# Kernel optimization log

Hardware: AMD Instinct MI355X
Metric: run time of the kernel (lower is better)

## Reference

```python
import jax, jax.numpy as jnp
import numpy as np

T, B, D_IN, D_H = 256, 256, 1024, 1024


def setup_inputs() -> dict:
    key = jax.random.key(0)
    k1, k2 = jax.random.split(key)
    seq = jax.random.normal(k1, (T, B, D_IN), dtype=jnp.float32)
    # Kaiming-ish init so tanh does not saturate
    W = jax.random.normal(k2, (D_H, D_IN + D_H), dtype=jnp.float32) / np.sqrt(D_IN + D_H)
    b = jnp.zeros((D_H,), dtype=jnp.float32)
    return {"seq": seq, "W": W, "b": b}


def reference(seq, W, b):
    # seq: (T, B, d_in); W: (d_h, d_in + d_h); b: (d_h,)
    d_h = W.shape[0]
    h0 = jnp.zeros((seq.shape[1], d_h), dtype=seq.dtype)

    def step(h, x):
        # h_{t+1} = tanh(W [h_t ; x_t] + b)
        h_new = jnp.tanh(jnp.concatenate([h, x], axis=-1) @ W.T + b)
        return h_new, h_new

    _, hs = jax.lax.scan(step, h0, seq)  # hs: (T, B, d_h)
    # Original returns the full hidden-state history including the initial zero state
    return jnp.concatenate([h0[None], hs], axis=0)  # (T+1, B, d_h)
```

## Files before the change

kernel.cpp:

```cpp
#include <hip/hip_runtime.h>

#define T_STEPS 256
#define BATCH   256
#define DIN     1024
#define DH      1024

typedef _Float16 half8_t __attribute__((ext_vector_type(8)));
typedef _Float16 half4_t __attribute__((ext_vector_type(4)));
typedef float    f32x4_t __attribute__((ext_vector_type(4)));

#define LDH  1032
#define REDW 68
#define LGW  72

#define CPOL_SYS 17

union H4U { half4_t h; unsigned long long u; };

__device__ __forceinline__ float ftanh(float x) {
    float t = x * 2.885390081777927f;
    float e = exp2f(t);
    float r = __builtin_amdgcn_rcpf(e + 1.0f);
    return 1.0f - 2.0f * r;
}

__global__ __launch_bounds__(256) void cvt_w(const float* __restrict__ W,
                                             _Float16* __restrict__ Wh,
                                             _Float16* __restrict__ Wx) {
    const int part = blockIdx.x >> 9;
    size_t base = ((size_t)(blockIdx.x & 511) * 256 + threadIdx.x) * 8;
    const int n = (int)(base >> 10);
    const int k = (int)(base & 1023);
    const float4* s = reinterpret_cast<const float4*>(W + (size_t)n * 2048 + part * 1024 + k);
    float4 a = s[0], b = s[1];
    half8_t h;
    h[0] = (_Float16)a.x; h[1] = (_Float16)a.y;
    h[2] = (_Float16)a.z; h[3] = (_Float16)a.w;
    h[4] = (_Float16)b.x; h[5] = (_Float16)b.y;
    h[6] = (_Float16)b.z; h[7] = (_Float16)b.w;
    _Float16* dst = part ? Wx : Wh;
    *reinterpret_cast<half8_t*>(dst + base) = h;
}

__global__ __launch_bounds__(256) void zero_h0(float* __restrict__ out,
                                               int* __restrict__ flags) {
    size_t i = (size_t)blockIdx.x * 256 + threadIdx.x;
    reinterpret_cast<float4*>(out)[i] = make_float4(0.f, 0.f, 0.f, 0.f);
    if (blockIdx.x == 0) {
#pragma unroll
        for (int j = 0; j < 16; ++j)
            __hip_atomic_store(&flags[(int)threadIdx.x * 16 + j], 0,
                               __ATOMIC_RELAXED, __HIP_MEMORY_SCOPE_SYSTEM);
    }
}

__global__ __launch_bounds__(256) void zgemm(const float* __restrict__ seq,
                                             const _Float16* __restrict__ Wx,
                                             const float* __restrict__ bias,
                                             float* __restrict__ out) {
    __shared__ __align__(16) _Float16 la[128 * LGW];
    __shared__ __align__(16) _Float16 lb[128 * LGW];

    const int tid  = threadIdx.x;
    const int id   = blockIdx.x;
    const int nblk = (id >> 3) & 7;
    const int mblk = (id & 7) + 8 * (id >> 6);
    const int m0 = mblk * 128;
    const int n0 = nblk * 128;

    const float* __restrict__ X = seq + (size_t)m0 * 1024;
    float* __restrict__ Z = out + (size_t)BATCH * DH + (size_t)m0 * 1024 + n0;

    const int ar = tid >> 1;
    const int kh = tid & 1;
    const float*    Asrc = X  + (size_t)ar * 1024 + kh * 32;
    const _Float16* Bsrc = Wx + (size_t)(n0 + ar) * 1024 + kh * 32;

    float4 af[8];
    uint4  bq[4];
    auto load_tiles = [&](int kb) {
        const float4* s4 = reinterpret_cast<const float4*>(Asrc + kb);
#pragma unroll
        for (int i = 0; i < 8; ++i) af[i] = s4[i];
        const uint4* sb = reinterpret_cast<const uint4*>(Bsrc + kb);
#pragma unroll
        for (int i = 0; i < 4; ++i) bq[i] = sb[i];
    };
    auto store_tiles = [&]() {
#pragma unroll
        for (int j = 0; j < 4; ++j) {
            half8_t h;
            h[0] = (_Float16)af[2 * j].x;     h[1] = (_Float16)af[2 * j].y;
            h[2] = (_Float16)af[2 * j].z;     h[3] = (_Float16)af[2 * j].w;
            h[4] = (_Float16)af[2 * j + 1].x; h[5] = (_Float16)af[2 * j + 1].y;
            h[6] = (_Float16)af[2 * j + 1].z; h[7] = (_Float16)af[2 * j + 1].w;
            *reinterpret_cast<half8_t*>(&la[ar * LGW + kh * 32 + j * 8]) = h;
        }
#pragma unroll
        for (int i = 0; i < 4; ++i)
            *reinterpret_cast<uint4*>(&lb[ar * LGW + kh * 32 + i * 8]) = bq[i];
    };

    const int wave = tid >> 6;
    const int lane = tid & 63;
    const int fr   = lane & 15;
    const int quad = lane >> 4;
    const int wm   = (wave >> 1) * 64;
    const int wn   = (wave & 1) * 64;

    f32x4_t acc[4][4];
#pragma unroll
    for (int i = 0; i < 4; ++i)
#pragma unroll
        for (int j = 0; j < 4; ++j) acc[i][j] = (f32x4_t){0.f, 0.f, 0.f, 0.f};

    load_tiles(0);
#pragma unroll 1
    for (int it = 0; it < 16; ++it) {
        store_tiles();
        __syncthreads();
        if (it < 15) load_tiles((it + 1) * 64);
#pragma unroll
        for (int kk = 0; kk < 2; ++kk) {
            const int ko = kk * 32 + quad * 8;
            half8_t a[4], b[4];
#pragma unroll
            for (int mi = 0; mi < 4; ++mi)
                a[mi] = *reinterpret_cast<const half8_t*>(
                    &la[(wm + mi * 16 + fr) * LGW + ko]);
#pragma unroll
            for (int ni = 0; ni < 4; ++ni)
                b[ni] = *reinterpret_cast<const half8_t*>(
                    &lb[(wn + ni * 16 + fr) * LGW + ko]);
#pragma unroll
            for (int mi = 0; mi < 4; ++mi)
#pragma unroll
                for (int ni = 0; ni < 4; ++ni)
                    acc[mi][ni] = __builtin_amdgcn_mfma_f32_16x16x32_f16(
                        a[mi], b[ni], acc[mi][ni], 0, 0, 0);
        }
        __syncthreads();
    }

#pragma unroll
    for (int ni = 0; ni < 4; ++ni) {
        const float bv = bias[n0 + wn + ni * 16 + fr];
#pragma unroll
        for (int mi = 0; mi < 4; ++mi) {
            const int mr = wm + mi * 16 + quad * 4;
#pragma unroll
            for (int q = 0; q < 4; ++q)
                Z[(size_t)(mr + q) * 1024 + wn + ni * 16 + fr] = acc[mi][ni][q] + bv;
        }
    }
}

__global__ __launch_bounds__(256, 1) void rnn_persist(
        const _Float16* __restrict__ Wh,
        _Float16* __restrict__ Hh,
        int* __restrict__ flags,
        float* __restrict__ out) {
    __shared__ __align__(16) _Float16 hL[16 * LDH];
    __shared__ __align__(16) float redL[16 * REDW];

    const int tid  = threadIdx.x;
    const int m    = blockIdx.x & 15;
    const int n    = blockIdx.x >> 4;
    const int wave = tid >> 6;
    const int lane = tid & 63;
    const int fr   = lane & 15;
    const int quad = lane >> 4;

    half8_t bfrag[32];
    {
        const _Float16* wp = Wh + (size_t)(n * 64 + wave * 16 + fr) * DH + quad * 8;
#pragma unroll
        for (int ks = 0; ks < 32; ++ks)
            bfrag[ks] = *reinterpret_cast<const half8_t*>(wp + ks * 32);
    }

    const int r  = tid >> 4;
    const int c4 = (tid & 15) * 4;
    const size_t orowg = (size_t)(m * 16 + r);
    int* myflag = flags + (m * 16 + n) * 16;

    {
        float* o1 = out + ((size_t)BATCH + orowg) * DH + n * 64 + c4;
        float4 z = *reinterpret_cast<const float4*>(o1);
        float4 v = make_float4(ftanh(z.x), ftanh(z.y), ftanh(z.z), ftanh(z.w));
        *reinterpret_cast<float4*>(o1) = v;
        H4U cv;
        cv.h[0] = (_Float16)v.x; cv.h[1] = (_Float16)v.y;
        cv.h[2] = (_Float16)v.z; cv.h[3] = (_Float16)v.w;
        __hip_atomic_store(
            (unsigned long long*)(Hh + ((size_t)BATCH + orowg) * DH + n * 64 + c4),
            cv.u, __ATOMIC_RELAXED, __HIP_MEMORY_SCOPE_SYSTEM);
        __syncthreads();
        if (tid == 0)
            __hip_atomic_store(myflag, 1, __ATOMIC_RELAXED, __HIP_MEMORY_SCOPE_SYSTEM);
    }

    for (int s = 1; s < T_STEPS; ++s) {
        float* o = out + ((size_t)(s + 1) * BATCH + orowg) * DH + n * 64 + c4;
        float4 z = *reinterpret_cast<const float4*>(o);

        if (tid < 16) {
            const int* f = flags + (m * 16 + tid) * 16;
            int guard = 0;
            while (__hip_atomic_load(f, __ATOMIC_RELAXED, __HIP_MEMORY_SCOPE_SYSTEM) < s) {
                if (++guard > (1 << 24)) break;
            }
        }
        __syncthreads();

        const _Float16* hsrc = Hh + ((size_t)(s & 1) * BATCH + (size_t)m * 16) * DH;
#pragma unroll
        for (int i = 0; i < 8; ++i) {
            const int c   = wave * 8 + i;
            const int row = c >> 1;
            const int hf  = c & 1;
            const _Float16* src = hsrc + (size_t)row * DH + hf * 512 + lane * 8;
            __builtin_amdgcn_global_load_lds(
                (const __attribute__((address_space(1))) void*)src,
                (__attribute__((address_space(3))) void*)&hL[row * LDH + hf * 512],
                16, 0, CPOL_SYS);
        }
        __syncthreads();

        f32x4_t acc0 = {0.f, 0.f, 0.f, 0.f}, acc1 = {0.f, 0.f, 0.f, 0.f};
        const _Float16* pa = &hL[fr * LDH + quad * 8];
#pragma unroll
        for (int ks = 0; ks < 16; ++ks) {
            half8_t ae = *reinterpret_cast<const half8_t*>(pa + (2 * ks) * 32);
            half8_t ao = *reinterpret_cast<const half8_t*>(pa + (2 * ks + 1) * 32);
            acc0 = __builtin_amdgcn_mfma_f32_16x16x32_f16(ae, bfrag[2 * ks],     acc0, 0, 0, 0);
            acc1 = __builtin_amdgcn_mfma_f32_16x16x32_f16(ao, bfrag[2 * ks + 1], acc1, 0, 0, 0);
        }
        f32x4_t sum = acc0 + acc1;

#pragma unroll
        for (int q = 0; q < 4; ++q)
            redL[(quad * 4 + q) * REDW + wave * 16 + fr] = sum[q];
        __syncthreads();

        f32x4_t t4 = *reinterpret_cast<const f32x4_t*>(&redL[r * REDW + c4]);
        float4 v = make_float4(ftanh(t4[0] + z.x), ftanh(t4[1] + z.y),
                               ftanh(t4[2] + z.z), ftanh(t4[3] + z.w));
        *reinterpret_cast<float4*>(o) = v;
        H4U cv;
        cv.h[0] = (_Float16)v.x; cv.h[1] = (_Float16)v.y;
        cv.h[2] = (_Float16)v.z; cv.h[3] = (_Float16)v.w;
        __hip_atomic_store(
            (unsigned long long*)(Hh + ((size_t)((s + 1) & 1) * BATCH + orowg) * DH
                                  + n * 64 + c4),
            cv.u, __ATOMIC_RELAXED, __HIP_MEMORY_SCOPE_SYSTEM);

        __syncthreads();
        if (tid == 0)
            __hip_atomic_store(myflag, s + 1, __ATOMIC_RELAXED, __HIP_MEMORY_SCOPE_SYSTEM);
    }
}

extern "C" void kernel_launch(void* const* d_in, const int* in_sizes, int n_in,
                              void* d_out, int out_size, void* d_ws, size_t ws_size,
                              hipStream_t stream) {
    const float* seq  = (const float*)d_in[0];
    const float* W    = (const float*)d_in[1];
    const float* bias = (const float*)d_in[2];
    float* out        = (float*)d_out;
    _Float16* Wh      = (_Float16*)d_ws;
    _Float16* Wx      = (_Float16*)d_ws + 1024 * 1024;
    _Float16* Hh      = (_Float16*)d_ws + 2 * 1024 * 1024;
    int* flags        = (int*)((char*)d_ws + 5 * 1024 * 1024);

    hipLaunchKernelGGL(cvt_w, dim3(1024), dim3(256), 0, stream, W, Wh, Wx);
    hipLaunchKernelGGL(zero_h0, dim3(256), dim3(256), 0, stream, out, flags);
    hipLaunchKernelGGL(zgemm, dim3(4096), dim3(256), 0, stream, seq, Wx, bias, out);
    hipLaunchKernelGGL(rnn_persist, dim3(256), dim3(256), 0, stream, Wh, Hh, flags, out);
}
```

Baseline: 1.542 ms.

## Fuse input-projection GEMM into persistent RNN kernel with per-tile readiness flags

Merges the input-projection GEMM and the persistent recurrent kernel into one launch. The first 256 blocks run the recurrence and the remaining 4096 blocks compute Z tiles, each publishing a ready flag. Recurrent blocks spin on the flag for the tile they need before reading Z, so the GEMM overlaps the sequential recurrence instead of running before it. This relies on the 256 persistent blocks being scheduled first and all staying resident. GEMM blocks now hold launch_bounds(256,1) and the larger shared-memory footprint, and Z stores and loads become system-scope atomics, which may cut GEMM throughput.

```diff
diff --git a/kernel.cpp b/kernel.cpp
--- a/kernel.cpp
+++ b/kernel.cpp
@@ -12,6 +12,7 @@
 #define LDH  1032
 #define REDW 68
 #define LGW  72
+#define LDS_BYTES 37376
 
 #define CPOL_SYS 17
 
@@ -43,7 +44,8 @@
 }
 
 __global__ __launch_bounds__(256) void zero_h0(float* __restrict__ out,
-                                               int* __restrict__ flags) {
+                                               int* __restrict__ flags,
+                                               int* __restrict__ zrdy) {
     size_t i = (size_t)blockIdx.x * 256 + threadIdx.x;
     reinterpret_cast<float4*>(out)[i] = make_float4(0.f, 0.f, 0.f, 0.f);
     if (blockIdx.x == 0) {
@@ -51,125 +53,138 @@
         for (int j = 0; j < 16; ++j)
             __hip_atomic_store(&flags[(int)threadIdx.x * 16 + j], 0,
                                __ATOMIC_RELAXED, __HIP_MEMORY_SCOPE_SYSTEM);
-    }
-}
-
-__global__ __launch_bounds__(256) void zgemm(const float* __restrict__ seq,
-                                             const _Float16* __restrict__ Wx,
-                                             const float* __restrict__ bias,
-                                             float* __restrict__ out) {
-    __shared__ __align__(16) _Float16 la[128 * LGW];
-    __shared__ __align__(16) _Float16 lb[128 * LGW];
-
-    const int tid  = threadIdx.x;
-    const int id   = blockIdx.x;
-    const int nblk = (id >> 3) & 7;
-    const int mblk = (id & 7) + 8 * (id >> 6);
-    const int m0 = mblk * 128;
-    const int n0 = nblk * 128;
-
-    const float* __restrict__ X = seq + (size_t)m0 * 1024;
-    float* __restrict__ Z = out + (size_t)BATCH * DH + (size_t)m0 * 1024 + n0;
-
-    const int ar = tid >> 1;
-    const int kh = tid & 1;
-    const float*    Asrc = X  + (size_t)ar * 1024 + kh * 32;
-    const _Float16* Bsrc = Wx + (size_t)(n0 + ar) * 1024 + kh * 32;
-
-    float4 af[8];
-    uint4  bq[4];
-    auto load_tiles = [&](int kb) {
-        const float4* s4 = reinterpret_cast<const float4*>(Asrc + kb);
-#pragma unroll
-        for (int i = 0; i < 8; ++i) af[i] = s4[i];
-        const uint4* sb = reinterpret_cast<const uint4*>(Bsrc + kb);
-#pragma unroll
-        for (int i = 0; i < 4; ++i) bq[i] = sb[i];
-    };
-    auto store_tiles = [&]() {
-#pragma unroll
-        for (int j = 0; j < 4; ++j) {
-            half8_t h;
-            h[0] = (_Float16)af[2 * j].x;     h[1] = (_Float16)af[2 * j].y;
-            h[2] = (_Float16)af[2 * j].z;     h[3] = (_Float16)af[2 * j].w;
-            h[4] = (_Float16)af[2 * j + 1].x; h[5] = (_Float16)af[2 * j + 1].y;
-            h[6] = (_Float16)af[2 * j + 1].z; h[7] = (_Float16)af[2 * j + 1].w;
-            *reinterpret_cast<half8_t*>(&la[ar * LGW + kh * 32 + j * 8]) = h;
-        }
-#pragma unroll
-        for (int i = 0; i < 4; ++i)
-            *reinterpret_cast<uint4*>(&lb[ar * LGW + kh * 32 + i * 8]) = bq[i];
-    };
+    } else if (blockIdx.x == 1) {
+#pragma unroll
+        for (int j = 0; j < 16; ++j)
+            __hip_atomic_store(&zrdy[(int)threadIdx.x * 16 + j], 0,
+                               __ATOMIC_RELAXED, __HIP_MEMORY_SCOPE_SYSTEM);
+    }
+}
+
+__global__ __launch_bounds__(256, 1) void fused_pipeline(
+        const _Float16* __restrict__ Wh,
+        const _Float16* __restrict__ Wx,
+        const float* __restrict__ bias,
+        const float* __restrict__ seq,
+        _Float16* __restrict__ Hh,
+        int* __restrict__ flags,
+        int* __restrict__ zrdy,
+        float* __restrict__ out) {
+    __shared__ __align__(16) char ldsraw[LDS_BYTES];
+    const int tid = threadIdx.x;
+    const int bid = blockIdx.x;
 
     const int wave = tid >> 6;
     const int lane = tid & 63;
     const int fr   = lane & 15;
     const int quad = lane >> 4;
-    const int wm   = (wave >> 1) * 64;
-    const int wn   = (wave & 1) * 64;
-
-    f32x4_t acc[4][4];
-#pragma unroll
-    for (int i = 0; i < 4; ++i)
-#pragma unroll
-        for (int j = 0; j < 4; ++j) acc[i][j] = (f32x4_t){0.f, 0.f, 0.f, 0.f};
-
-    load_tiles(0);
+
+    if (bid >= 256) {
+        _Float16* la = reinterpret_cast<_Float16*>(ldsraw);
+        _Float16* lb = la + 128 * LGW;
+
+        const int id   = bid - 256;
+        const int nblk = (id >> 3) & 7;
+        const int mblk = (id & 7) + 8 * (id >> 6);
+        const int m0 = mblk * 128;
+        const int n0 = nblk * 128;
+
+        const float* __restrict__ X = seq + (size_t)m0 * 1024;
+        float* __restrict__ Z = out + (size_t)BATCH * DH + (size_t)m0 * 1024 + n0;
+
+        const int ar = tid >> 1;
+        const int kh = tid & 1;
+        const float*    Asrc = X  + (size_t)ar * 1024 + kh * 32;
+        const _Float16* Bsrc = Wx + (size_t)(n0 + ar) * 1024 + kh * 32;
+
+        float4 af[8];
+        uint4  bq[4];
+        auto load_tiles = [&](int kb) {
+            const float4* s4 = reinterpret_cast<const float4*>(Asrc + kb);
+#pragma unroll
+            for (int i = 0; i < 8; ++i) af[i] = s4[i];
+            const uint4* sb = reinterpret_cast<const uint4*>(Bsrc + kb);
+#pragma unroll
+            for (int i = 0; i < 4; ++i) bq[i] = sb[i];
+        };
+        auto store_tiles = [&]() {
+#pragma unroll
+            for (int j = 0; j < 4; ++j) {
+                half8_t h;
+                h[0] = (_Float16)af[2 * j].x;     h[1] = (_Float16)af[2 * j].y;
+                h[2] = (_Float16)af[2 * j].z;     h[3] = (_Float16)af[2 * j].w;
+                h[4] = (_Float16)af[2 * j + 1].x; h[5] = (_Float16)af[2 * j + 1].y;
+                h[6] = (_Float16)af[2 * j + 1].z; h[7] = (_Float16)af[2 * j + 1].w;
+                *reinterpret_cast<half8_t*>(&la[ar * LGW + kh * 32 + j * 8]) = h;
+            }
+#pragma unroll
+            for (int i = 0; i < 4; ++i)
+                *reinterpret_cast<uint4*>(&lb[ar * LGW + kh * 32 + i * 8]) = bq[i];
+        };
+
+        const int wm = (wave >> 1) * 64;
+        const int wn = (wave & 1) * 64;
+
+        f32x4_t acc[4][4];
+#pragma unroll
+        for (int i = 0; i < 4; ++i)
+#pragma unroll
+            for (int j = 0; j < 4; ++j) acc[i][j] = (f32x4_t){0.f, 0.f, 0.f, 0.f};
+
+        load_tiles(0);
 #pragma unroll 1
-    for (int it = 0; it < 16; ++it) {
-        store_tiles();
-        __syncthreads();
-        if (it < 15) load_tiles((it + 1) * 64);
-#pragma unroll
-        for (int kk = 0; kk < 2; ++kk) {
-            const int ko = kk * 32 + quad * 8;
-            half8_t a[4], b[4];
-#pragma unroll
-            for (int mi = 0; mi < 4; ++mi)
-                a[mi] = *reinterpret_cast<const half8_t*>(
-                    &la[(wm + mi * 16 + fr) * LGW + ko]);
-#pragma unroll
-            for (int ni = 0; ni < 4; ++ni)
-                b[ni] = *reinterpret_cast<const half8_t*>(
-                    &lb[(wn + ni * 16 + fr) * LGW + ko]);
-#pragma unroll
-            for (int mi = 0; mi < 4; ++mi)
+        for (int it = 0; it < 16; ++it) {
+            store_tiles();
+            __syncthreads();
+            if (it < 15) load_tiles((it + 1) * 64);
+#pragma unroll
+            for (int kk = 0; kk < 2; ++kk) {
+                const int ko = kk * 32 + quad * 8;
+                half8_t a[4], b[4];
+#pragma unroll
+                for (int mi = 0; mi < 4; ++mi)
+                    a[mi] = *reinterpret_cast<const half8_t*>(
+                        &la[(wm + mi * 16 + fr) * LGW + ko]);
 #pragma unroll
                 for (int ni = 0; ni < 4; ++ni)
-                    acc[mi][ni] = __builtin_amdgcn_mfma_f32_16x16x32_f16(
-                        a[mi], b[ni], acc[mi][ni], 0, 0, 0);
-        }
-        __syncthreads();
-    }
-
-#pragma unroll
-    for (int ni = 0; ni < 4; ++ni) {
-        const float bv = bias[n0 + wn + ni * 16 + fr];
-#pragma unroll
-        for (int mi = 0; mi < 4; ++mi) {
-            const int mr = wm + mi * 16 + quad * 4;
-#pragma unroll
-            for (int q = 0; q < 4; ++q)
-                Z[(size_t)(mr + q) * 1024 + wn + ni * 16 + fr] = acc[mi][ni][q] + bv;
-        }
-    }
-}
-
-__global__ __launch_bounds__(256, 1) void rnn_persist(
-        const _Float16* __restrict__ Wh,
-        _Float16* __restrict__ Hh,
-        int* __restrict__ flags,
-        float* __restrict__ out) {
-    __shared__ __align__(16) _Float16 hL[16 * LDH];
-    __shared__ __align__(16) float redL[16 * REDW];
-
-    const int tid  = threadIdx.x;
-    const int m    = blockIdx.x & 15;
-    const int n    = blockIdx.x >> 4;
-    const int wave = tid >> 6;
-    const int lane = tid & 63;
-    const int fr   = lane & 15;
-    const int quad = lane >> 4;
+                    b[ni] = *reinterpret_cast<const half8_t*>(
+                        &lb[(wn + ni * 16 + fr) * LGW + ko]);
+#pragma unroll
+                for (int mi = 0; mi < 4; ++mi)
+#pragma unroll
+                    for (int ni = 0; ni < 4; ++ni)
+                        acc[mi][ni] = __builtin_amdgcn_mfma_f32_16x16x32_f16(
+                            a[mi], b[ni], acc[mi][ni], 0, 0, 0);
+            }
+            __syncthreads();
+        }
+
+#pragma unroll
+        for (int ni = 0; ni < 4; ++ni) {
+            const float bv = bias[n0 + wn + ni * 16 + fr];
+#pragma unroll
+            for (int mi = 0; mi < 4; ++mi) {
+                const int mr = wm + mi * 16 + quad * 4;
+#pragma unroll
+                for (int q = 0; q < 4; ++q)
+                    __hip_atomic_store(
+                        &Z[(size_t)(mr + q) * 1024 + wn + ni * 16 + fr],
+                        acc[mi][ni][q] + bv,
+                        __ATOMIC_RELAXED, __HIP_MEMORY_SCOPE_SYSTEM);
+            }
+        }
+        __syncthreads();
+        if (tid == 0)
+            __hip_atomic_store(&zrdy[mblk * 8 + nblk], 1,
+                               __ATOMIC_RELAXED, __HIP_MEMORY_SCOPE_SYSTEM);
+        return;
+    }
+
+    _Float16* hL   = reinterpret_cast<_Float16*>(ldsraw);
+    float*    redL = reinterpret_cast<float*>(ldsraw + 16 * LDH * 2);
+
+    const int m = bid & 15;
+    const int n = bid >> 4;
 
     half8_t bfrag[32];
     {
@@ -183,11 +198,28 @@
     const int c4 = (tid & 15) * 4;
     const size_t orowg = (size_t)(m * 16 + r);
     int* myflag = flags + (m * 16 + n) * 16;
+    const int zcol = n >> 1;
+    const int mhalf = m >> 3;
 
     {
+        if (tid == 0) {
+            const int* zf = zrdy + (0 + mhalf) * 8 + zcol;
+            int g = 0;
+            while (!__hip_atomic_load(zf, __ATOMIC_RELAXED,
+                                      __HIP_MEMORY_SCOPE_SYSTEM)) {
+                if (++g > (1 << 25)) break;
+            }
+        }
+        __syncthreads();
+
         float* o1 = out + ((size_t)BATCH + orowg) * DH + n * 64 + c4;
-        float4 z = *reinterpret_cast<const float4*>(o1);
-        float4 v = make_float4(ftanh(z.x), ftanh(z.y), ftanh(z.z), ftanh(z.w));
+        float zv[4];
+#pragma unroll
+        for (int j = 0; j < 4; ++j)
+            zv[j] = __hip_atomic_load(o1 + j, __ATOMIC_RELAXED,
+                                      __HIP_MEMORY_SCOPE_SYSTEM);
+        float4 v = make_float4(ftanh(zv[0]), ftanh(zv[1]),
+                               ftanh(zv[2]), ftanh(zv[3]));
         *reinterpret_cast<float4*>(o1) = v;
         H4U cv;
         cv.h[0] = (_Float16)v.x; cv.h[1] = (_Float16)v.y;
@@ -201,14 +233,19 @@
     }
 
     for (int s = 1; s < T_STEPS; ++s) {
-        float* o = out + ((size_t)(s + 1) * BATCH + orowg) * DH + n * 64 + c4;
-        float4 z = *reinterpret_cast<const float4*>(o);
-
         if (tid < 16) {
             const int* f = flags + (m * 16 + tid) * 16;
             int guard = 0;
-            while (__hip_atomic_load(f, __ATOMIC_RELAXED, __HIP_MEMORY_SCOPE_SYSTEM) < s) {
-                if (++guard > (1 << 24)) break;
+            while (__hip_atomic_load(f, __ATOMIC_RELAXED,
+                                     __HIP_MEMORY_SCOPE_SYSTEM) < s) {
+                if (++guard > (1 << 25)) break;
+            }
+        } else if (tid == 16) {
+            const int* zf = zrdy + (2 * s + mhalf) * 8 + zcol;
+            int guard = 0;
+            while (!__hip_atomic_load(zf, __ATOMIC_RELAXED,
+                                      __HIP_MEMORY_SCOPE_SYSTEM)) {
+                if (++guard > (1 << 25)) break;
             }
         }
         __syncthreads();
@@ -225,6 +262,12 @@
                 (__attribute__((address_space(3))) void*)&hL[row * LDH + hf * 512],
                 16, 0, CPOL_SYS);
         }
+        float* o = out + ((size_t)(s + 1) * BATCH + orowg) * DH + n * 64 + c4;
+        float zv[4];
+#pragma unroll
+        for (int j = 0; j < 4; ++j)
+            zv[j] = __hip_atomic_load(o + j, __ATOMIC_RELAXED,
+                                      __HIP_MEMORY_SCOPE_SYSTEM);
         __syncthreads();
 
         f32x4_t acc0 = {0.f, 0.f, 0.f, 0.f}, acc1 = {0.f, 0.f, 0.f, 0.f};
@@ -244,8 +287,8 @@
         __syncthreads();
 
         f32x4_t t4 = *reinterpret_cast<const f32x4_t*>(&redL[r * REDW + c4]);
-        float4 v = make_float4(ftanh(t4[0] + z.x), ftanh(t4[1] + z.y),
-                               ftanh(t4[2] + z.z), ftanh(t4[3] + z.w));
+        float4 v = make_float4(ftanh(t4[0] + zv[0]), ftanh(t4[1] + zv[1]),
+                               ftanh(t4[2] + zv[2]), ftanh(t4[3] + zv[3]));
         *reinterpret_cast<float4*>(o) = v;
         H4U cv;
         cv.h[0] = (_Float16)v.x; cv.h[1] = (_Float16)v.y;
@@ -272,9 +315,10 @@
     _Float16* Wx      = (_Float16*)d_ws + 1024 * 1024;
     _Float16* Hh      = (_Float16*)d_ws + 2 * 1024 * 1024;
     int* flags        = (int*)((char*)d_ws + 5 * 1024 * 1024);
+    int* zrdy         = (int*)((char*)d_ws + 5 * 1024 * 1024 + 16 * 1024);
 
     hipLaunchKernelGGL(cvt_w, dim3(1024), dim3(256), 0, stream, W, Wh, Wx);
-    hipLaunchKernelGGL(zero_h0, dim3(256), dim3(256), 0, stream, out, flags);
-    hipLaunchKernelGGL(zgemm, dim3(4096), dim3(256), 0, stream, seq, Wx, bias, out);
-    hipLaunchKernelGGL(rnn_persist, dim3(256), dim3(256), 0, stream, Wh, Hh, flags, out);
-}
+    hipLaunchKernelGGL(zero_h0, dim3(256), dim3(256), 0, stream, out, flags, zrdy);
+    hipLaunchKernelGGL(fused_pipeline, dim3(256 + 4096), dim3(256), 0, stream,
+                       Wh, Wx, bias, seq, Hh, flags, zrdy, out);
+}
```

Result: faster. 1.333 ms (-13.6%).
